# Kernel tuning notes

Hardware: AMD Instinct MI355X
Metric: run time of the kernel (lower is better)

## Reference

```python
import jax, jax.numpy as jnp
import numpy as np
from jax import lax

CONF_TH = 0.4     # confidence_threshold (module default self.confidence)
IOU_TH = 0.45     # iou_threshold
MAX_WH = 4096.0   # class offset for non-agnostic NMS
K = 2048          # fixed candidate capacity (analog of max_nms cap)
MAX_DET = 300     # max detections kept per image
NC = 80           # number of classes


def xywh2xyxy(b):
    # b: [..., 4] center-x, center-y, w, h -> x1, y1, x2, y2
    xy, wh = b[..., :2], b[..., 2:]
    return jnp.concatenate([xy - wh * 0.5, xy + wh * 0.5], axis=-1)


def pairwise_iou(boxes):
    # boxes: [K, 4] xyxy -> [K, K] IoU
    area = (boxes[:, 2] - boxes[:, 0]) * (boxes[:, 3] - boxes[:, 1])
    lt = jnp.maximum(boxes[:, None, :2], boxes[None, :, :2])
    rb = jnp.minimum(boxes[:, None, 2:], boxes[None, :, 2:])
    wh = jnp.clip(rb - lt, 0.0)
    inter = wh[..., 0] * wh[..., 1]
    return inter / (area[:, None] + area[None, :] - inter + 1e-7)


def _nms_one(pred, log_):
    # pred: [N, 5+NC], log_: [N, NC]
    obj = pred[:, 4]
    cls_scores = pred[:, 5:] * obj[:, None]          # x[:, 5:] *= x[:, 4:5]
    box = xywh2xyxy(pred[:, :4])
    conf = jnp.max(cls_scores, axis=1)               # conf, j = x[:, 5:].max(1)
    j = jnp.argmax(cls_scores, axis=1)
    valid = (obj > CONF_TH) & (conf > CONF_TH)       # xc mask then conf filter
    score = jnp.where(valid, conf, -1.0)

    # take top-K candidates by score (sorted descending, like argsort cap)
    top_score, top_idx = lax.top_k(score, K)         # [K]
    valid_k = top_score > 0.0
    top_box = box[top_idx]                           # [K, 4] original coords
    top_cls = j[top_idx].astype(pred.dtype)          # [K]
    top_log = log_[top_idx]                          # [K, NC]

    # class-offset boxes for non-agnostic NMS
    off_box = top_box + (top_cls * MAX_WH)[:, None]
    iou = pairwise_iou(off_box)                      # [K, K]

    # greedy suppression in score order (candidates already sorted desc)
    ar = jnp.arange(K)

    def body(i, supp):
        alive = valid_k[i] & jnp.logical_not(supp[i])
        return supp | (alive & (iou[i] > IOU_TH) & (ar > i))

    supp = lax.fori_loop(0, K, body, jnp.zeros((K,), bool))
    keep = valid_k & jnp.logical_not(supp)

    # scatter first MAX_DET kept rows into fixed-size output slots
    rank = jnp.cumsum(keep.astype(jnp.int32)) - 1
    slot = jnp.where(keep & (rank < MAX_DET), rank, MAX_DET)  # MAX_DET = dump row
    rows = jnp.concatenate(
        [top_box, top_score[:, None], top_cls[:, None]], axis=1)  # [K, 6]
    dets = jnp.zeros((MAX_DET + 1, 6), pred.dtype).at[slot].set(rows)[:MAX_DET]
    logs = jnp.zeros((MAX_DET + 1, NC), pred.dtype).at[slot].set(top_log)[:MAX_DET]
    return jnp.concatenate([dets, logs], axis=1)     # [MAX_DET, 6+NC]


def setup_inputs() -> dict:
    key = jax.random.key(0)
    k1, k2, k3, k4, k5 = jax.random.split(key, 5)
    B, N = 16, 25200
    xy = jax.random.uniform(k1, (B, N, 2), jnp.float32) * 640.0
    wh = jax.random.uniform(k2, (B, N, 2), jnp.float32) * 120.0 + 4.0
    obj = jax.random.uniform(k3, (B, N, 1), jnp.float32)
    cls = jax.random.uniform(k4, (B, N, NC), jnp.float32)
    prediction = jnp.concatenate([xy, wh, obj, cls], axis=-1)  # [B, N, 85]
    logits = jax.random.normal(k5, (B, N, NC), jnp.float32)
    return {"prediction": prediction, "logits": logits}


def reference(prediction, logits):
    # returns padded detections+logits: [B, MAX_DET, 6+NC]
    # columns 0:4 = xyxy, 4 = conf, 5 = class, 6: = pruned logits; empty slots are 0
    return jax.vmap(_nms_one)(prediction, logits)
```

## Files before the change

kernel.cpp:

```cpp
#include <hip/hip_runtime.h>
#include <stdint.h>

#define BATCH 16
#define NDET 25200
#define NCLS 80
#define PREDC 85
#define KTOP 2048
#define MAXDET 300
#define OUTC 86
#define CONF_THR 0.4f
#define IOU_THR 0.45f
#define MAXWH 4096.0f
#define INVHI 0xBF800000u
#define BMW (NCLS * 64)
#define NB 8192
#define QPB ((MAXDET * OUTC) / 4)
#define BPB ((QPB + 255) / 256)

typedef float fx4 __attribute__((ext_vector_type(4)));

__device__ __forceinline__ uint32_t mono_f32(float f) {
  uint32_t u = __float_as_uint(f);
  return (u & 0x80000000u) ? ~u : (u | 0x80000000u);
}
__device__ __forceinline__ float unmono_f32(uint32_t m) {
  uint32_t u = (m & 0x80000000u) ? (m & 0x7FFFFFFFu) : ~m;
  return __uint_as_float(u);
}

__global__ void __launch_bounds__(256) k_keys(const float* __restrict__ pred,
                                              uint32_t* __restrict__ sw,
                                              uint8_t* __restrict__ cls8) {
  int gq = blockIdx.x * 64 + (threadIdx.x >> 2);
  int q = threadIdx.x & 3;
  const float* row = pred + (size_t)gq * PREDC;
  float obj = row[4];
  float score = -1.0f;
  uint32_t cl = 0;
  if (obj > CONF_THR) {
    float best = -1e30f;
    int bc = 0;
#pragma unroll
    for (int k = 0; k < 5; ++k) {
#pragma unroll
      for (int j = 0; j < 4; ++j) {
        int c = k * 16 + q * 4 + j;
        float s = __fmul_rn(row[5 + c], obj);
        if (s > best) { best = s; bc = c; }
      }
    }
    for (int d = 1; d <= 2; d <<= 1) {
      float vo = __shfl_xor(best, d);
      int co = __shfl_xor(bc, d);
      if (vo > best || (vo == best && co < bc)) { best = vo; bc = co; }
    }
    if (best > CONF_THR) { score = best; cl = (uint32_t)bc; }
  }
  if (q == 0) {
    sw[gq] = ~mono_f32(score);
    cls8[gq] = (uint8_t)cl;
  }
}

__global__ void __launch_bounds__(1024) k_sel(
    const uint32_t* __restrict__ sw, const uint8_t* __restrict__ cls8,
    const float* __restrict__ pred,
    uint32_t* __restrict__ s_n, float* __restrict__ s_score, float* __restrict__ s_clsf,
    uint32_t* __restrict__ clsbm, float* __restrict__ s_box, float* __restrict__ s_obox,
    uint32_t* __restrict__ keepbm) {
  __shared__ uint64_t sk[KTOP];
  __shared__ uint32_t hist[NB];
  __shared__ uint32_t seg[64];
  __shared__ uint32_t sh_digit, sh_cnt, sh_k;
  __shared__ uint32_t ncol;
  int b = blockIdx.x, tid = threadIdx.x, lane = tid & 63;
  const uint32_t* swb = sw + (size_t)b * NDET;
  const uint8_t* clb = cls8 + (size_t)b * NDET;
  const uint4* sw4 = (const uint4*)swb;
  if (tid == 0) { sh_k = KTOP; ncol = 0; }
  if (tid < 64) keepbm[b * 64 + tid] = 0;

#define CLEAR_HIST() { __syncthreads(); \
  for (int i = tid; i < NB; i += 1024) hist[i] = 0; \
  __syncthreads(); }

#define FIND() { __syncthreads(); \
  if (tid < 64) { uint32_t s_ = 0; \
    for (int i_ = 0; i_ < NB / 64; ++i_) s_ += hist[tid * (NB / 64) + i_]; \
    seg[tid] = s_; } \
  __syncthreads(); \
  if (tid == 0) { uint32_t k_ = sh_k, cum_ = 0; int S_ = 0; \
    for (; S_ < 63; ++S_) { if (cum_ + seg[S_] >= k_) break; cum_ += seg[S_]; } \
    int d_ = S_ * (NB / 64); \
    for (;; ++d_) { if (cum_ + hist[d_] >= k_) break; cum_ += hist[d_]; } \
    sh_digit = (uint32_t)d_; sh_cnt = hist[d_]; sh_k = k_ - cum_; } \
  __syncthreads(); }

  CLEAR_HIST();
  {
    uint32_t invc = 0;
#define PA(s) { if ((s) == INVHI) ++invc; \
    else atomicAdd(&hist[((s) - 0x40000000u) >> 13], 1u); }
    for (int i = tid; i < NDET / 4; i += 1024) {
      uint4 v = sw4[i];
      PA(v.x) PA(v.y) PA(v.z) PA(v.w)
    }
    if (invc) atomicAdd(&hist[NB - 1], invc);
  }
  FIND();
  uint32_t dA = sh_digit;
  uint32_t sstar, E, r, Lstar = 0xFFFFFFFFu;
  if (dA == NB - 1) {
    sstar = INVHI; E = sh_cnt; r = sh_k;
  } else {
    CLEAR_HIST();
    for (int i = tid; i < NDET / 4; i += 1024) {
      uint4 v = sw4[i];
#define PB(s) { if ((s) != INVHI && (((s) - 0x40000000u) >> 13) == dA) \
      atomicAdd(&hist[(s) & 0x1FFFu], 1u); }
      PB(v.x) PB(v.y) PB(v.z) PB(v.w)
    }
    FIND();
    sstar = 0x40000000u + (dA << 13) + sh_digit;
    E = sh_cnt; r = sh_k;
  }

  if (r < E) {
    CLEAR_HIST();
    for (int n = tid; n < NDET; n += 1024) {
      if (swb[n] == sstar) {
        uint32_t low = ((uint32_t)n << 7) | clb[n];
        atomicAdd(&hist[low >> 11], 1u);
      }
    }
    FIND();
    uint32_t dr0 = sh_digit;
    CLEAR_HIST();
    for (int n = tid; n < NDET; n += 1024) {
      if (swb[n] == sstar) {
        uint32_t low = ((uint32_t)n << 7) | clb[n];
        if ((low >> 11) == dr0) atomicAdd(&hist[low & 0x7FFu], 1u);
      }
    }
    FIND();
    Lstar = (dr0 << 11) | sh_digit;
  }

  for (int n = tid; n < NDET; n += 1024) {
    uint32_t hi = swb[n];
    uint32_t low = 0;
    bool inc = false;
    if (hi < sstar) inc = true;
    else if (hi == sstar) { low = ((uint32_t)n << 7) | clb[n]; inc = (low <= Lstar); }
    uint64_t ball = __ballot(inc);
    uint32_t bse = 0;
    if (lane == 0) bse = atomicAdd(&ncol, (uint32_t)__popcll(ball));
    bse = __shfl(bse, 0);
    if (inc) {
      if (hi < sstar) low = ((uint32_t)n << 7) | clb[n];
      uint32_t pos = bse + (uint32_t)__popcll(ball & ((1ull << lane) - 1ull));
      if (pos < KTOP) sk[pos] = ((uint64_t)hi << 32) | low;
    }
  }
  __syncthreads();

  {
    int wv = tid >> 6, ln = tid & 63;
    int i1 = wv * 128 + ln;
    int i2 = i1 + 64;
    uint64_t lo = sk[i1], hi = sk[i2];

#define CMPEX_SHFL(j, kk) { \
      uint64_t plo = __shfl_xor((unsigned long long)lo, (j)); \
      uint64_t phi = __shfl_xor((unsigned long long)hi, (j)); \
      bool low1 = ((ln & (j)) == 0); \
      bool km1 = (low1 == ((i1 & (kk)) == 0)); \
      lo = km1 ? (lo < plo ? lo : plo) : (lo > plo ? lo : plo); \
      bool km2 = (low1 == ((i2 & (kk)) == 0)); \
      hi = km2 ? (hi < phi ? hi : phi) : (hi > phi ? hi : phi); }
#define CMPEX_LANE(kk) { \
      bool asc_ = ((i1 & (kk)) == 0); \
      uint64_t mn = lo < hi ? lo : hi; \
      uint64_t mx = lo < hi ? hi : lo; \
      lo = asc_ ? mn : mx; hi = asc_ ? mx : mn; }

    for (int kk = 2; kk <= 128; kk <<= 1) {
      for (int j = kk >> 1; j > 0; j >>= 1) {
        if (j == 64) { CMPEX_LANE(kk) }
        else CMPEX_SHFL(j, kk)
      }
    }
    for (int kk = 256; kk <= KTOP; kk <<= 1) {
      for (int j = kk >> 1; j >= 128; j >>= 1) {
        sk[i1] = lo; sk[i2] = hi;
        __syncthreads();
        uint64_t p1 = sk[i1 ^ j], p2 = sk[i2 ^ j];
        bool km1 = (((i1 & j) == 0) == ((i1 & kk) == 0));
        lo = km1 ? (lo < p1 ? lo : p1) : (lo > p1 ? lo : p1);
        bool km2 = (((i2 & j) == 0) == ((i2 & kk) == 0));
        hi = km2 ? (hi < p2 ? hi : p2) : (hi > p2 ? hi : p2);
        __syncthreads();
      }
      for (int j = 64; j > 0; j >>= 1) {
        if (j == 64) { CMPEX_LANE(kk) }
        else CMPEX_SHFL(j, kk)
      }
    }
    sk[i1] = lo; sk[i2] = hi;
  }
  __syncthreads();

  uint32_t* bm = hist;
  for (int i = tid; i < BMW; i += 1024) bm[i] = 0;
  __syncthreads();

  for (int rr = tid; rr < KTOP; rr += 1024) {
    uint64_t key = sk[rr];
    float score = unmono_f32(~(uint32_t)(key >> 32));
    uint32_t low = (uint32_t)key;
    uint32_t n = low >> 7;
    uint32_t cls = low & 127u;
    if (score > 0.0f) atomicOr(&bm[cls * 64 + (rr >> 5)], 1u << (rr & 31));
    const float* p = pred + ((size_t)b * NDET + n) * PREDC;
    float x = p[0], y = p[1], w = p[2], h = p[3];
    float hw = __fmul_rn(w, 0.5f), hh = __fmul_rn(h, 0.5f);
    float x1 = __fsub_rn(x, hw), y1 = __fsub_rn(y, hh);
    float x2 = __fadd_rn(x, hw), y2 = __fadd_rn(y, hh);
    float clsf = (float)cls;
    float off = __fmul_rn(clsf, MAXWH);
    size_t o = (size_t)b * KTOP + rr;
    s_n[o] = n;
    s_score[o] = score;
    s_clsf[o] = clsf;
    s_box[o * 4 + 0] = x1; s_box[o * 4 + 1] = y1;
    s_box[o * 4 + 2] = x2; s_box[o * 4 + 3] = y2;
    s_obox[o * 4 + 0] = __fadd_rn(x1, off); s_obox[o * 4 + 1] = __fadd_rn(y1, off);
    s_obox[o * 4 + 2] = __fadd_rn(x2, off); s_obox[o * 4 + 3] = __fadd_rn(y2, off);
  }
  __syncthreads();
  for (int i = tid; i < BMW; i += 1024) clsbm[(size_t)b * BMW + i] = bm[i];
}

__global__ void __launch_bounds__(64) k_cnms(
    const uint32_t* __restrict__ clsbm, const float* __restrict__ s_obox,
    uint32_t* __restrict__ keepbm) {
  __shared__ uint16_t memb[KTOP];
  __shared__ float bx1[KTOP], by1[KTOP], bx2[KTOP], by2[KTOP];
  __shared__ uint64_t aliveM[KTOP / 64];
  int b = blockIdx.x / NCLS, c = blockIdx.x % NCLS;
  int lane = threadIdx.x;
  uint32_t w = clsbm[(size_t)b * BMW + c * 64 + lane];
  int cnt = __popc(w);
  int scan = cnt;
  for (int d = 1; d < 64; d <<= 1) {
    int v = __shfl_up(scan, d);
    if (lane >= d) scan += v;
  }
  int m = __shfl(scan, 63);
  if (m == 0) return;
  int p = scan - cnt;
  uint32_t ww = w;
  while (ww) { int t = __ffs(ww) - 1; ww &= ww - 1; memb[p++] = (uint16_t)(lane * 32 + t); }
  __syncthreads();
  for (int i = lane; i < m; i += 64) {
    const float* bp = s_obox + ((size_t)b * KTOP + memb[i]) * 4;
    bx1[i] = bp[0]; by1[i] = bp[1]; bx2[i] = bp[2]; by2[i] = bp[3];
  }
  __syncthreads();
  int nch = (m + 63) >> 6;
  for (int ch = 0; ch < nch; ++ch) {
    int base = ch * 64;
    int my = base + lane;
    bool has = my < m;
    float ax1 = 0, ay1 = 0, ax2 = 0, ay2 = 0, aarea = 0;
    if (has) {
      ax1 = bx1[my]; ay1 = by1[my]; ax2 = bx2[my]; ay2 = by2[my];
      aarea = __fmul_rn(__fsub_rn(ax2, ax1), __fsub_rn(ay2, ay1));
    }
    bool supp = false;
#define IOU_SUPP(j, guard) { \
      float jx1 = bx1[j], jy1 = by1[j], jx2 = bx2[j], jy2 = by2[j]; \
      float jarea = __fmul_rn(__fsub_rn(jx2, jx1), __fsub_rn(jy2, jy1)); \
      float ltx = fmaxf(jx1, ax1), lty = fmaxf(jy1, ay1); \
      float rbx = fminf(jx2, ax2), rby = fminf(jy2, ay2); \
      float wx = fmaxf(__fsub_rn(rbx, ltx), 0.0f); \
      float wy = fmaxf(__fsub_rn(rby, lty), 0.0f); \
      float inter = __fmul_rn(wx, wy); \
      float denom = __fadd_rn(__fsub_rn(__fadd_rn(jarea, aarea), inter), 1e-7f); \
      float iou = __fdiv_rn(inter, denom); \
      supp = supp || ((guard) && iou > IOU_THR); }
    for (int pc = 0; pc < ch; ++pc) {
      uint64_t aw = aliveM[pc];
      while (aw) {
        int e = __ffsll((unsigned long long)aw) - 1; aw &= aw - 1;
        int j = pc * 64 + e;
        IOU_SUPP(j, has)
      }
    }
    uint64_t sm = __ballot(supp);
    int csz = (m - base >= 64) ? 64 : (m - base);
    for (int d = 0; d < csz; ++d) {
      if (!((sm >> d) & 1ull)) {
        int j = base + d;
        IOU_SUPP(j, (lane > d) && has)
        sm = __ballot(supp);
      }
    }
    uint64_t vmask = (csz == 64) ? ~0ull : ((1ull << csz) - 1ull);
    if (lane == 0) aliveM[ch] = (~sm) & vmask;
    __syncthreads();
    if (has && !supp) {
      int rk = memb[my];
      atomicOr(&keepbm[b * 64 + (rk >> 5)], 1u << (rk & 31));
    }
  }
}

__global__ void __launch_bounds__(256) k_outw(
    const uint32_t* __restrict__ keepbm, const uint32_t* __restrict__ s_n,
    const float* __restrict__ s_score, const float* __restrict__ s_clsf,
    const float* __restrict__ s_box, const float* __restrict__ logits,
    fx4* __restrict__ dout) {
  __shared__ int src[MAXDET];
  int b = blockIdx.x / BPB;
  int jb = blockIdx.x % BPB;
  int tid = threadIdx.x;
  for (int s = tid; s < MAXDET; s += 256) src[s] = -1;
  __syncthreads();
  if (tid < 64) {
    uint32_t keep = keepbm[b * 64 + tid];
    uint32_t cnt = __popc(keep);
    uint32_t scan = cnt;
    for (int d = 1; d < 64; d <<= 1) {
      uint32_t v = __shfl_up(scan, d);
      if (tid >= d) scan += v;
    }
    uint32_t pfx = scan - cnt;
    int lo = tid * 32;
    while (keep) {
      int t = __ffs(keep) - 1;
      keep &= keep - 1;
      if (pfx < MAXDET) src[pfx] = lo + t;
      ++pfx;
    }
  }
  __syncthreads();
  int i = jb * 256 + tid;
  if (i >= QPB) return;
  float v0, v1, v2, v3;
#define GETV(k, dst) { \
    int idx = i * 4 + k; \
    int slot = idx / OUTC; \
    int c = idx - slot * OUTC; \
    int r = src[slot]; \
    float x = 0.0f; \
    if (r >= 0) { \
      size_t o = (size_t)b * KTOP + r; \
      if (c < 4) x = s_box[o * 4 + c]; \
      else if (c == 4) x = s_score[o]; \
      else if (c == 5) x = s_clsf[o]; \
      else x = logits[((size_t)b * NDET + s_n[o]) * NCLS + (c - 6)]; \
    } \
    dst = x; }
  GETV(0, v0) GETV(1, v1) GETV(2, v2) GETV(3, v3)
  fx4 f4 = {v0, v1, v2, v3};
  __builtin_nontemporal_store(f4, &dout[(size_t)b * QPB + i]);
}

extern "C" void kernel_launch(void* const* d_in, const int* in_sizes, int n_in,
                              void* d_out, int out_size, void* d_ws, size_t ws_size,
                              hipStream_t stream) {
  const float* pred = (const float*)d_in[0];
  const float* logits = (const float*)d_in[1];

  char* ws = (char*)d_ws;
  size_t off = 0;
  auto alloc = [&](size_t bytes) -> void* {
    void* p = ws + off;
    off += (bytes + 255) & ~(size_t)255;
    return p;
  };
  uint32_t* sw    = (uint32_t*)alloc((size_t)BATCH * NDET * 4);
  uint8_t*  cls8  = (uint8_t*)alloc((size_t)BATCH * NDET);
  uint32_t* s_n   = (uint32_t*)alloc((size_t)BATCH * KTOP * 4);
  float*    s_sc  = (float*)alloc((size_t)BATCH * KTOP * 4);
  float*    s_cl  = (float*)alloc((size_t)BATCH * KTOP * 4);
  uint32_t* clsbm = (uint32_t*)alloc((size_t)BATCH * BMW * 4);
  float*    s_box = (float*)alloc((size_t)BATCH * KTOP * 16);
  float*    s_ob  = (float*)alloc((size_t)BATCH * KTOP * 16);
  uint32_t* keepb = (uint32_t*)alloc((size_t)BATCH * 64 * 4);
  (void)ws_size; (void)in_sizes; (void)n_in;

  k_keys<<<(BATCH * NDET) / 64, 256, 0, stream>>>(pred, sw, cls8);
  k_sel<<<BATCH, 1024, 0, stream>>>(sw, cls8, pred, s_n, s_sc, s_cl, clsbm, s_box, s_ob, keepb);
  k_cnms<<<BATCH * NCLS, 64, 0, stream>>>(clsbm, s_ob, keepb);
  k_outw<<<BATCH * BPB, 256, 0, stream>>>(keepb, s_n, s_sc, s_cl, s_box, logits, (fx4*)d_out);
}
```

Before: 100.5 us.

## Build coarse score histogram in key kernel and rank the boundary bin directly

```diff
diff --git a/kernel.cpp b/kernel.cpp
--- a/kernel.cpp
+++ b/kernel.cpp
@@ -14,6 +14,7 @@
 #define INVHI 0xBF800000u
 #define BMW (NCLS * 64)
 #define NB 8192
+#define SIDECAP 2048
 #define QPB ((MAXDET * OUTC) / 4)
 #define BPB ((QPB + 255) / 256)
 
@@ -30,7 +31,11 @@
 
 __global__ void __launch_bounds__(256) k_keys(const float* __restrict__ pred,
                                               uint32_t* __restrict__ sw,
-                                              uint8_t* __restrict__ cls8) {
+                                              uint8_t* __restrict__ cls8,
+                                              uint32_t* __restrict__ histA) {
+  __shared__ uint32_t invc[2];
+  if (threadIdx.x < 2) invc[threadIdx.x] = 0;
+  __syncthreads();
   int gq = blockIdx.x * 64 + (threadIdx.x >> 2);
   int q = threadIdx.x & 3;
   const float* row = pred + (size_t)gq * PREDC;
@@ -56,110 +61,109 @@
     }
     if (best > CONF_THR) { score = best; cl = (uint32_t)bc; }
   }
+  int b = gq / NDET;
+  int b0 = (blockIdx.x * 64) / NDET;
   if (q == 0) {
-    sw[gq] = ~mono_f32(score);
+    uint32_t hi = ~mono_f32(score);
+    sw[gq] = hi;
     cls8[gq] = (uint8_t)cl;
+    if (score > 0.0f)
+      atomicAdd(&histA[(size_t)b * NB + ((hi - 0x40000000u) >> 13)], 1u);
+    else
+      atomicAdd(&invc[b - b0], 1u);
+  }
+  __syncthreads();
+  if (threadIdx.x < 2) {
+    uint32_t c = invc[threadIdx.x];
+    if (c) atomicAdd(&histA[(size_t)(b0 + threadIdx.x) * NB + (NB - 1)], c);
   }
 }
 
 __global__ void __launch_bounds__(1024) k_sel(
     const uint32_t* __restrict__ sw, const uint8_t* __restrict__ cls8,
-    const float* __restrict__ pred,
+    const float* __restrict__ pred, const uint32_t* __restrict__ histA,
     uint32_t* __restrict__ s_n, float* __restrict__ s_score, float* __restrict__ s_clsf,
     uint32_t* __restrict__ clsbm, float* __restrict__ s_box, float* __restrict__ s_obox,
     uint32_t* __restrict__ keepbm) {
   __shared__ uint64_t sk[KTOP];
+  __shared__ uint64_t side[SIDECAP];
   __shared__ uint32_t hist[NB];
-  __shared__ uint32_t seg[64];
-  __shared__ uint32_t sh_digit, sh_cnt, sh_k;
-  __shared__ uint32_t ncol;
+  __shared__ uint32_t sh_dA, ncolM, ncolS;
   int b = blockIdx.x, tid = threadIdx.x, lane = tid & 63;
   const uint32_t* swb = sw + (size_t)b * NDET;
   const uint8_t* clb = cls8 + (size_t)b * NDET;
-  const uint4* sw4 = (const uint4*)swb;
-  if (tid == 0) { sh_k = KTOP; ncol = 0; }
+  const uint32_t* ha = histA + (size_t)b * NB;
+  for (int i = tid; i < NB; i += 1024) hist[i] = ha[i];
+  if (tid == 0) { ncolM = 0; ncolS = 0; }
   if (tid < 64) keepbm[b * 64 + tid] = 0;
-
-#define CLEAR_HIST() { __syncthreads(); \
-  for (int i = tid; i < NB; i += 1024) hist[i] = 0; \
-  __syncthreads(); }
-
-#define FIND() { __syncthreads(); \
-  if (tid < 64) { uint32_t s_ = 0; \
-    for (int i_ = 0; i_ < NB / 64; ++i_) s_ += hist[tid * (NB / 64) + i_]; \
-    seg[tid] = s_; } \
-  __syncthreads(); \
-  if (tid == 0) { uint32_t k_ = sh_k, cum_ = 0; int S_ = 0; \
-    for (; S_ < 63; ++S_) { if (cum_ + seg[S_] >= k_) break; cum_ += seg[S_]; } \
-    int d_ = S_ * (NB / 64); \
-    for (;; ++d_) { if (cum_ + hist[d_] >= k_) break; cum_ += hist[d_]; } \
-    sh_digit = (uint32_t)d_; sh_cnt = hist[d_]; sh_k = k_ - cum_; } \
-  __syncthreads(); }
-
-  CLEAR_HIST();
-  {
-    uint32_t invc = 0;
-#define PA(s) { if ((s) == INVHI) ++invc; \
-    else atomicAdd(&hist[((s) - 0x40000000u) >> 13], 1u); }
-    for (int i = tid; i < NDET / 4; i += 1024) {
-      uint4 v = sw4[i];
-      PA(v.x) PA(v.y) PA(v.z) PA(v.w)
-    }
-    if (invc) atomicAdd(&hist[NB - 1], invc);
-  }
-  FIND();
-  uint32_t dA = sh_digit;
-  uint32_t sstar, E, r, Lstar = 0xFFFFFFFFu;
-  if (dA == NB - 1) {
-    sstar = INVHI; E = sh_cnt; r = sh_k;
-  } else {
-    CLEAR_HIST();
-    for (int i = tid; i < NDET / 4; i += 1024) {
-      uint4 v = sw4[i];
-#define PB(s) { if ((s) != INVHI && (((s) - 0x40000000u) >> 13) == dA) \
-      atomicAdd(&hist[(s) & 0x1FFFu], 1u); }
-      PB(v.x) PB(v.y) PB(v.z) PB(v.w)
-    }
-    FIND();
-    sstar = 0x40000000u + (dA << 13) + sh_digit;
-    E = sh_cnt; r = sh_k;
-  }
-
-  if (r < E) {
-    CLEAR_HIST();
-    for (int n = tid; n < NDET; n += 1024) {
-      if (swb[n] == sstar) {
-        uint32_t low = ((uint32_t)n << 7) | clb[n];
-        atomicAdd(&hist[low >> 11], 1u);
-      }
-    }
-    FIND();
-    uint32_t dr0 = sh_digit;
-    CLEAR_HIST();
-    for (int n = tid; n < NDET; n += 1024) {
-      if (swb[n] == sstar) {
-        uint32_t low = ((uint32_t)n << 7) | clb[n];
-        if ((low >> 11) == dr0) atomicAdd(&hist[low & 0x7FFu], 1u);
-      }
-    }
-    FIND();
-    Lstar = (dr0 << 11) | sh_digit;
-  }
+  __syncthreads();
+
+  if (tid < 64) {
+    uint32_t segsum = 0;
+    for (int i = 0; i < NB / 64; ++i) segsum += hist[lane * (NB / 64) + i];
+    uint32_t scan = segsum;
+    for (int d = 1; d < 64; d <<= 1) { uint32_t v = __shfl_up(scan, d); if (lane >= d) scan += v; }
+    uint32_t excl = scan - segsum;
+    bool win = (excl < KTOP) && (KTOP <= scan);
+    uint64_t wb = __ballot(win);
+    int S = __ffsll((unsigned long long)wb) - 1;
+    uint32_t kRem = KTOP - __shfl(excl, S);
+    uint32_t v0 = hist[S * (NB / 64) + lane];
+    uint32_t v1 = hist[S * (NB / 64) + 64 + lane];
+    uint32_t s0 = v0;
+    for (int d = 1; d < 64; d <<= 1) { uint32_t v = __shfl_up(s0, d); if (lane >= d) s0 += v; }
+    uint32_t tot0 = __shfl(s0, 63);
+    uint32_t e0 = s0 - v0;
+    uint32_t s1 = v1;
+    for (int d = 1; d < 64; d <<= 1) { uint32_t v = __shfl_up(s1, d); if (lane >= d) s1 += v; }
+    uint32_t e1 = s1 - v1 + tot0;
+    bool w0 = (e0 < kRem) && (kRem <= e0 + v0);
+    bool w1 = (e1 < kRem) && (kRem <= e1 + v1);
+    uint64_t b0m = __ballot(w0), b1m = __ballot(w1);
+    int dA;
+    if (b0m) dA = S * (NB / 64) + (__ffsll((unsigned long long)b0m) - 1);
+    else     dA = S * (NB / 64) + 64 + (__ffsll((unsigned long long)b1m) - 1);
+    if (lane == 0) sh_dA = (uint32_t)dA;
+  }
+  __syncthreads();
+  uint32_t dA = sh_dA;
 
   for (int n = tid; n < NDET; n += 1024) {
     uint32_t hi = swb[n];
-    uint32_t low = 0;
-    bool inc = false;
-    if (hi < sstar) inc = true;
-    else if (hi == sstar) { low = ((uint32_t)n << 7) | clb[n]; inc = (low <= Lstar); }
-    uint64_t ball = __ballot(inc);
-    uint32_t bse = 0;
-    if (lane == 0) bse = atomicAdd(&ncol, (uint32_t)__popcll(ball));
-    bse = __shfl(bse, 0);
-    if (inc) {
-      if (hi < sstar) low = ((uint32_t)n << 7) | clb[n];
-      uint32_t pos = bse + (uint32_t)__popcll(ball & ((1ull << lane) - 1ull));
-      if (pos < KTOP) sk[pos] = ((uint64_t)hi << 32) | low;
+    uint32_t bin = (hi != INVHI) ? ((hi - 0x40000000u) >> 13) : (NB - 1);
+    bool mp = (bin < dA);
+    bool sp = (bin == dA);
+    uint64_t bm_ = __ballot(mp);
+    uint64_t bs_ = __ballot(sp);
+    uint32_t baseM = 0, baseS = 0;
+    if (lane == 0) {
+      if (bm_) baseM = atomicAdd(&ncolM, (uint32_t)__popcll(bm_));
+      if (bs_) baseS = atomicAdd(&ncolS, (uint32_t)__popcll(bs_));
+    }
+    baseM = __shfl(baseM, 0);
+    baseS = __shfl(baseS, 0);
+    uint64_t lmask = (1ull << lane) - 1ull;
+    if (mp) {
+      uint64_t key = ((uint64_t)hi << 32) | (((uint32_t)n << 7) | clb[n]);
+      sk[baseM + (uint32_t)__popcll(bm_ & lmask)] = key;
+    }
+    if (sp) {
+      uint64_t key = ((uint64_t)hi << 32) | (((uint32_t)n << 7) | clb[n]);
+      uint32_t p = baseS + (uint32_t)__popcll(bs_ & lmask);
+      if (p < SIDECAP) side[p] = key;
+    }
+  }
+  __syncthreads();
+
+  {
+    uint32_t C = ncolM;
+    uint32_t s = ncolS; if (s > SIDECAP) s = SIDECAP;
+    uint32_t rp = KTOP - C;
+    for (uint32_t i = tid; i < s; i += 1024) {
+      uint64_t ki = side[i];
+      uint32_t rk = 0;
+      for (uint32_t j = 0; j < s; ++j) rk += (side[j] < ki) ? 1u : 0u;
+      if (rk < rp) sk[C + rk] = ki;
     }
   }
   __syncthreads();
@@ -382,6 +386,7 @@
   };
   uint32_t* sw    = (uint32_t*)alloc((size_t)BATCH * NDET * 4);
   uint8_t*  cls8  = (uint8_t*)alloc((size_t)BATCH * NDET);
+  uint32_t* histA = (uint32_t*)alloc((size_t)BATCH * NB * 4);
   uint32_t* s_n   = (uint32_t*)alloc((size_t)BATCH * KTOP * 4);
   float*    s_sc  = (float*)alloc((size_t)BATCH * KTOP * 4);
   float*    s_cl  = (float*)alloc((size_t)BATCH * KTOP * 4);
@@ -391,8 +396,9 @@
   uint32_t* keepb = (uint32_t*)alloc((size_t)BATCH * 64 * 4);
   (void)ws_size; (void)in_sizes; (void)n_in;
 
-  k_keys<<<(BATCH * NDET) / 64, 256, 0, stream>>>(pred, sw, cls8);
-  k_sel<<<BATCH, 1024, 0, stream>>>(sw, cls8, pred, s_n, s_sc, s_cl, clsbm, s_box, s_ob, keepb);
+  hipMemsetAsync(histA, 0, (size_t)BATCH * NB * 4, stream);
+  k_keys<<<(BATCH * NDET) / 64, 256, 0, stream>>>(pred, sw, cls8, histA);
+  k_sel<<<BATCH, 1024, 0, stream>>>(sw, cls8, pred, histA, s_n, s_sc, s_cl, clsbm, s_box, s_ob, keepb);
   k_cnms<<<BATCH * NCLS, 64, 0, stream>>>(clsbm, s_ob, keepb);
   k_outw<<<BATCH * BPB, 256, 0, stream>>>(keepb, s_n, s_sc, s_cl, s_box, logits, (fx4*)d_out);
 }
```

Measured after the change: 130.7 us. 1.3x slower.
